# Performance work log

Hardware: AMD Instinct MI355X
Metric: run time of the kernel (lower is better)

The kernel has to match this reference:

```python
import jax, jax.numpy as jnp
import numpy as np

NHEADS = 16
LN_EPS = 1e-5


def setup_inputs() -> dict:
    key = jax.random.key(0)
    ks = jax.random.split(key, 12)
    B, L, D = 8, 1024, 1024
    bound = 1.0 / np.sqrt(D)
    inp = {
        'query': jax.random.normal(ks[0], (B, L, D), jnp.float32),
        'key':   jax.random.normal(ks[1], (B, L, D), jnp.float32),
        'value': jax.random.normal(ks[2], (B, L, D), jnp.float32),
        'q_mask': jnp.ones((B, L), jnp.float32),
        'k_mask': jnp.ones((B, L), jnp.float32),
        'Wq': jax.random.uniform(ks[3], (D, D), jnp.float32, -bound, bound),
        'bq': jax.random.uniform(ks[4], (D,), jnp.float32, -bound, bound),
        'Wk': jax.random.uniform(ks[5], (D, D), jnp.float32, -bound, bound),
        'bk': jax.random.uniform(ks[6], (D,), jnp.float32, -bound, bound),
        'Wv': jax.random.uniform(ks[7], (D, D), jnp.float32, -bound, bound),
        'bv': jax.random.uniform(ks[8], (D,), jnp.float32, -bound, bound),
        'Wo': jax.random.uniform(ks[9], (D, D), jnp.float32, -bound, bound),
        'bo': jax.random.uniform(ks[10], (D,), jnp.float32, -bound, bound),
        'gamma': jnp.ones((D,), jnp.float32),
        'beta': jnp.zeros((D,), jnp.float32),
    }
    return inp


def reference(query, key, value, q_mask, k_mask, Wq, bq, Wk, bk, Wv, bv, Wo, bo, gamma, beta):
    B, L, D = query.shape
    H = NHEADS
    d = D // H
    residual = query
    # linear projections (torch Linear: x @ W.T + b)
    q = query @ Wq.T + bq
    k = key @ Wk.T + bk
    v = value @ Wv.T + bv
    # NOTE: module does a raw contiguous view [B, L, H*d] -> [B*H, L, d]
    # (NOT a transpose-based head split). Replicate exactly.
    q = q.reshape(B * H, L, d)
    k = k.reshape(B * H, L, d)
    v = v.reshape(B * H, L, d)
    # masks tiled head-major: repeat(nheads, 1) -> [H*B, L]
    qm = jnp.tile(q_mask, (H, 1))
    km = jnp.tile(k_mask, (H, 1))
    mask = qm[:, :, None] * km[:, None, :]  # [B*H, L, L] outer product
    scores = jnp.einsum('bqd,bkd->bqk', q, k) / np.sqrt(d).astype(np.float32)
    A = jnp.exp(jnp.where(mask == 0, -jnp.inf, scores))  # unstable exp, as in source
    A_sum = jnp.clip(jnp.sum(A, axis=-1, keepdims=True), 2e-15, None)
    attn = A / A_sum
    context = (attn @ v).reshape(B, L, H * d)
    out = context @ Wo.T + bo
    # dropout is identity in eval mode
    x = residual + out
    mean = jnp.mean(x, axis=-1, keepdims=True)
    var = jnp.mean(jnp.square(x - mean), axis=-1, keepdims=True)
    return (x - mean) / jnp.sqrt(var + LN_EPS) * gamma + beta
```

## Files before the change

kernel.cpp:

```cpp
#include <hip/hip_runtime.h>
#include <hip/hip_bf16.h>


typedef __bf16 bf16x8 __attribute__((ext_vector_type(8)));
typedef float  f32x4  __attribute__((ext_vector_type(4)));

#define KK 1024
#define NN 1024

union BfPack4 { __bf16 h[4]; uint2 u; };
union BfPack8 { __bf16 h[8]; uint4 u; };

__device__ int g_nomask;

__device__ __forceinline__ void lds_copy16(void* lds, const void* gsrc) {
  __builtin_amdgcn_global_load_lds(
      (__attribute__((address_space(1))) void*)(uintptr_t)gsrc,
      (__attribute__((address_space(3))) void*)(unsigned int)(uintptr_t)lds,
      16, 0, 0);
}

struct Prep {
  const float* wsrc[4]; __bf16* wdst;
  const float* asrc[3]; __bf16* adst; int do_a;
  const float* qm; const float* km;
};

__global__ __launch_bounds__(256) void prep_kernel(Prep a) {
  const int bid = blockIdx.x;
  const int tid = threadIdx.x;
  if (bid < 12288) {
    if (!a.do_a) return;
    const int z = bid >> 12, i = bid & 4095;
    const float* s = a.asrc[z];
    __bf16* d = a.adst + (size_t)z * ((size_t)8 << 20);
    const size_t off = ((size_t)i * 256 + tid) * 8;
    float4 f0 = *(const float4*)&s[off];
    float4 f1 = *(const float4*)&s[off + 4];
    BfPack8 p;
    p.h[0] = (__bf16)f0.x; p.h[1] = (__bf16)f0.y;
    p.h[2] = (__bf16)f0.z; p.h[3] = (__bf16)f0.w;
    p.h[4] = (__bf16)f1.x; p.h[5] = (__bf16)f1.y;
    p.h[6] = (__bf16)f1.z; p.h[7] = (__bf16)f1.w;
    *(uint4*)&d[off] = p.u;
  } else if (bid < 16384) {
    const int b = bid - 12288;
    const int z = b >> 10, i = b & 1023;
    const float* s = a.wsrc[z];
    __bf16* d = a.wdst + (size_t)z * (KK * NN);
    const int idx = (i * 256 + tid) * 4;
    float4 f = *(const float4*)&s[idx];
    BfPack4 p;
    p.h[0] = (__bf16)f.x; p.h[1] = (__bf16)f.y;
    p.h[2] = (__bf16)f.z; p.h[3] = (__bf16)f.w;
    *(uint2*)&d[idx] = p.u;
  } else {
    int ok = 1;
    for (int i = tid; i < 8192; i += 256)
      ok &= (a.qm[i] != 0.f) & (a.km[i] != 0.f);
    const int all_ok = __syncthreads_and(ok);
    if (tid == 0) g_nomask = all_ok;
  }
}

struct G8 {
  const __bf16* A[3];
  const __bf16* W[3];
  const float*  bias[3];
  void*         C[3];
};

#define BAR()   __builtin_amdgcn_s_barrier()
#define PRIO(x) __builtin_amdgcn_s_setprio(x)
#define WAIT_LGKM0() do { asm volatile("s_waitcnt lgkmcnt(0)" ::: "memory"); \
                          __builtin_amdgcn_sched_barrier(0); } while (0)
#define WAIT_VM4()  asm volatile("s_waitcnt vmcnt(4)" ::: "memory")
#define WAIT_VM0()  asm volatile("s_waitcnt vmcnt(0)" ::: "memory")

#define STAGE_A(buf, half, kt) do {                                          \
  lds_copy16(smem + (buf)*32768 + (half)*16384 + ldsW,                       \
             pA0[half] + (size_t)(kt)*64);                                   \
  lds_copy16(smem + (buf)*32768 + (half)*16384 + ldsW + 1024,                \
             pA1[half] + (size_t)(kt)*64); } while (0)

#define STAGE_B(buf, half, kt) do {                                          \
  lds_copy16(smem + 65536 + (buf)*32768 + (half)*16384 + ldsW,               \
             pB0[half] + (size_t)(kt)*64);                                   \
  lds_copy16(smem + 65536 + (buf)*32768 + (half)*16384 + ldsW + 1024,        \
             pB1[half] + (size_t)(kt)*64); } while (0)

#define LDA(buf, mh) do {                                                    \
  const char* _p = aSelf + (buf)*32768 + (mh)*8192;                          \
  _Pragma("unroll") for (int i_ = 0; i_ < 4; ++i_) {                         \
    af[i_][0] = *(const bf16x8*)(_p + i_*2048 + c0_);                        \
    af[i_][1] = *(const bf16x8*)(_p + i_*2048 + c1_); } } while (0)

#define LDB(buf, nh) do {                                                    \
  const char* _p = bSelf + (buf)*32768 + (nh)*4096;                          \
  _Pragma("unroll") for (int j_ = 0; j_ < 2; ++j_) {                         \
    bf[(nh)*2 + j_][0] = *(const bf16x8*)(_p + j_*2048 + c0_);               \
    bf[(nh)*2 + j_][1] = *(const bf16x8*)(_p + j_*2048 + c1_); } } while (0)

#define MM(mh, nh) do {                                                      \
  _Pragma("unroll") for (int i_ = 0; i_ < 4; ++i_)                           \
  _Pragma("unroll") for (int j_ = 0; j_ < 2; ++j_) {                         \
    acc[(mh)*4+i_][(nh)*2+j_] = __builtin_amdgcn_mfma_f32_16x16x32_bf16(     \
        af[i_][0], bf[(nh)*2+j_][0], acc[(mh)*4+i_][(nh)*2+j_], 0, 0, 0);    \
    acc[(mh)*4+i_][(nh)*2+j_] = __builtin_amdgcn_mfma_f32_16x16x32_bf16(     \
        af[i_][1], bf[(nh)*2+j_][1], acc[(mh)*4+i_][(nh)*2+j_], 0, 0, 0);    \
  } } while (0)

template <bool OUT_BF16>
__global__ __launch_bounds__(512, 2) void gemm8p(G8 args)
{
  __shared__ __align__(16) char smem[131072];
  const int z = blockIdx.z;
  const __bf16* __restrict__ A    = args.A[z];
  const __bf16* __restrict__ W    = args.W[z];
  const float*  __restrict__ bias = args.bias[z];

  const int tid = threadIdx.x;
  const int l = tid & 63, w = tid >> 6;
  const int lr = l & 15, lq = l >> 4;
  const int wr = w >> 2, wc = w & 3;

  int lin = blockIdx.y * 32 + blockIdx.x;
  lin = (lin & 7) * 16 + (lin >> 3);
  const int m0 = (lin & 31) * 256;
  const int n0 = (lin >> 5) * 256;

  const int s0 = w * 128 + l, s1 = s0 + 64;
  const int r0 = s0 >> 3, kq0 = (s0 & 7) ^ (r0 & 7);
  const int r1 = s1 >> 3, kq1 = (s1 & 7) ^ (r1 & 7);
  const __bf16* pA0[2]; const __bf16* pA1[2];
  const __bf16* pB0[2]; const __bf16* pB1[2];
  #pragma unroll
  for (int h = 0; h < 2; ++h) {
    pA0[h] = A + (size_t)(m0 + h * 128 + r0) * KK + kq0 * 8;
    pA1[h] = A + (size_t)(m0 + h * 128 + r1) * KK + kq1 * 8;
    pB0[h] = W + (size_t)(n0 + h * 128 + r0) * KK + kq0 * 8;
    pB1[h] = W + (size_t)(n0 + h * 128 + r1) * KK + kq1 * 8;
  }
  const int ldsW = w * 2048;

  const int aRow = lr * 128;
  const int c0_ = ((lq)     ^ (lr & 7)) * 16;
  const int c1_ = ((4 + lq) ^ (lr & 7)) * 16;
  const char* aSelf = smem + wr * 16384 + aRow;
  const char* bSelf = smem + 65536 + (wc >> 1) * 16384 + (wc & 1) * 8192 + aRow;

  bf16x8 af[4][2], bf[4][2];
  f32x4 acc[8][4] = {};

  STAGE_A(0, 0, 0); STAGE_A(0, 1, 0);
  STAGE_B(0, 0, 0); STAGE_B(0, 1, 0);
  STAGE_B(1, 0, 1); STAGE_B(1, 1, 1);
  WAIT_VM4();
  BAR();

  for (int it = 0; it < 8; ++it) {
    const int t2 = it * 2;
    LDA(0, 0); LDB(0, 0);
    STAGE_A(1, 0, t2 + 1);
    BAR(); WAIT_LGKM0();
    PRIO(1); MM(0, 0); PRIO(0);
    BAR();
    LDB(0, 1);
    STAGE_A(1, 1, t2 + 1);
    BAR(); WAIT_LGKM0();
    PRIO(1); MM(0, 1); PRIO(0);
    BAR();
    LDA(0, 1);
    if (it < 7) STAGE_B(0, 0, t2 + 2);
    BAR(); WAIT_LGKM0();
    PRIO(1); MM(1, 0); PRIO(0);
    BAR();
    if (it < 7) { STAGE_B(0, 1, t2 + 2); WAIT_VM4(); }
    else        { WAIT_VM0(); }
    BAR();
    PRIO(1); MM(1, 1); PRIO(0);
    BAR();
    LDA(1, 0); LDB(1, 0);
    if (it < 7) STAGE_A(0, 0, t2 + 2);
    BAR(); WAIT_LGKM0();
    PRIO(1); MM(0, 0); PRIO(0);
    BAR();
    LDB(1, 1);
    if (it < 7) STAGE_A(0, 1, t2 + 2);
    BAR(); WAIT_LGKM0();
    PRIO(1); MM(0, 1); PRIO(0);
    BAR();
    LDA(1, 1);
    if (it < 7) STAGE_B(1, 0, t2 + 3);
    BAR(); WAIT_LGKM0();
    PRIO(1); MM(1, 0); PRIO(0);
    BAR();
    if (it < 7) { STAGE_B(1, 1, t2 + 3); WAIT_VM4(); }
    BAR();
    PRIO(1); MM(1, 1); PRIO(0);
    BAR();
  }

  float bv[4];
  #pragma unroll
  for (int n = 0; n < 4; ++n) bv[n] = bias[n0 + wc * 64 + n * 16 + lr];

  #pragma unroll
  for (int f = 0; f < 8; ++f) {
    const int gm = m0 + wr * 128 + f * 16 + lq * 4;
    #pragma unroll
    for (int n = 0; n < 4; ++n) {
      const int gn = n0 + wc * 64 + n * 16 + lr;
      #pragma unroll
      for (int i = 0; i < 4; ++i) {
        const float v = acc[f][n][i] + bv[n];
        if constexpr (OUT_BF16)
          ((__bf16*)args.C[z])[(size_t)(gm + i) * NN + gn] = (__bf16)v;
        else
          ((float*)args.C[z])[(size_t)(gm + i) * NN + gn] = v;
      }
    }
  }
}

struct GQKV {
  const float*  A[3];
  const __bf16* W;
  const float*  bias[3];
  __bf16*       C[3];
};

__global__ __launch_bounds__(256) void gemm_qkv(GQKV args)
{
  __shared__ alignas(16) __bf16 As[128 * 40];
  __shared__ alignas(16) __bf16 Bs[2][4096];
  const int z = blockIdx.z;
  const float*  A    = args.A[z];
  const __bf16* W    = args.W + (size_t)z * KK * NN;
  const float*  bias = args.bias[z];
  __bf16* C = args.C[z];
  const int tid = threadIdx.x, l = tid & 63, w = tid >> 6;
  const int m0 = blockIdx.x * 128, n0 = blockIdx.y * 128;
  const int lr = l & 15, lq = l >> 4;
  const int wm = (w & 1) * 64, wn = (w >> 1) * 64;

  const __bf16* gw0 = &W[(size_t)(n0 + (tid >> 2)) * KK + (tid & 3) * 8];
  const __bf16* gw1 = &W[(size_t)(n0 + 64 + (tid >> 2)) * KK + (tid & 3) * 8];

  float4 pa[4];
  #pragma unroll
  for (int s = 0; s < 4; ++s) {
    int c = tid + 256 * s; int row = c >> 3, ko = (c & 7) * 4;
    pa[s] = *(const float4*)&A[(size_t)(m0 + row) * KK + ko];
  }
  lds_copy16((char*)Bs + w * 1024,        gw0);
  lds_copy16((char*)Bs + 4096 + w * 1024, gw1);

  f32x4 acc[4][4] = {};
  int ib = 0;
  for (int kk = 0; kk < KK; kk += 32) {
    __syncthreads();
    #pragma unroll
    for (int s = 0; s < 4; ++s) {
      int c = tid + 256 * s; int row = c >> 3, ko = (c & 7) * 4;
      BfPack4 p;
      p.h[0] = (__bf16)pa[s].x; p.h[1] = (__bf16)pa[s].y;
      p.h[2] = (__bf16)pa[s].z; p.h[3] = (__bf16)pa[s].w;
      *(uint2*)&As[row * 40 + ko] = p.u;
    }
    __syncthreads();
    if (kk + 32 < KK) {
      lds_copy16((char*)Bs + (ib ^ 1) * 8192 + w * 1024,        gw0 + kk + 32);
      lds_copy16((char*)Bs + (ib ^ 1) * 8192 + 4096 + w * 1024, gw1 + kk + 32);
      #pragma unroll
      for (int s = 0; s < 4; ++s) {
        int c = tid + 256 * s; int row = c >> 3, ko = (c & 7) * 4;
        pa[s] = *(const float4*)&A[(size_t)(m0 + row) * KK + kk + 32 + ko];
      }
    }
    const __bf16* Bb = (const __bf16*)((char*)Bs + ib * 8192);
    bf16x8 af2[4], bf2[4];
    #pragma unroll
    for (int t = 0; t < 4; ++t) {
      af2[t] = *(const bf16x8*)&As[(wm + t * 16 + lr) * 40 + lq * 8];
      bf2[t] = *(const bf16x8*)&Bb[(wn + t * 16 + lr) * 32 + lq * 8];
    }
    #pragma unroll
    for (int mt = 0; mt < 4; ++mt)
      #pragma unroll
      for (int nt = 0; nt < 4; ++nt)
        acc[mt][nt] = __builtin_amdgcn_mfma_f32_16x16x32_bf16(af2[mt], bf2[nt], acc[mt][nt], 0, 0, 0);
    ib ^= 1;
  }

  #pragma unroll
  for (int mt = 0; mt < 4; ++mt)
    #pragma unroll
    for (int nt = 0; nt < 4; ++nt)
      #pragma unroll
      for (int i = 0; i < 4; ++i) {
        int gm = m0 + wm + mt * 16 + lq * 4 + i;
        int gn = n0 + wn + nt * 16 + lr;
        C[(size_t)gm * NN + gn] = (__bf16)(acc[mt][nt][i] + bias[gn]);
      }
}

__global__ __launch_bounds__(256) void attn_kernel(
    const __bf16* __restrict__ qb, const __bf16* __restrict__ kb,
    const __bf16* __restrict__ vb, const float* __restrict__ qm,
    const float* __restrict__ km, __bf16* __restrict__ ctxb)
{
  const int g  = blockIdx.x * 16 + (blockIdx.y >> 3);
  const int qt = blockIdx.y & 7;
  const int tid = threadIdx.x, l = tid & 63, w = tid >> 6;
  const int lr = l & 15, lq = l >> 4;

  __shared__ alignas(16) __bf16 Ps[128 * 64];
  __shared__ alignas(16) __bf16 Ks[2 * 128 * 32];
  __shared__ alignas(16) __bf16 Vt[64 * 128];
  __shared__ alignas(16) __bf16 kms[1024];

  const size_t gbase = (size_t)g * (1024 * 64);
  const __bf16* qg = qb + gbase;
  const __bf16* kg = kb + gbase;
  const __bf16* vg = vb + gbase;
  const float* qmrow = qm + (size_t)(g & 7) * 1024;
  const float* kmrow = km + (size_t)(g & 7) * 1024;
  const int nm = g_nomask;

  #pragma unroll
  for (int s = 0; s < 4; ++s) {
    int c = tid + 256 * s;
    int p = c >> 9, r = (c >> 2) & 127, q0 = c & 3;
    lds_copy16((char*)Ps + w * 1024 + s * 4096,
               &qg[(size_t)(qt * 128 + r) * 64 + p * 32 + q0 * 8]);
  }
  {
    float4 kf = *(const float4*)&kmrow[tid * 4];
    BfPack4 p;
    p.h[0] = (__bf16)(kf.x == 0.f ? 0.f : 1.f);
    p.h[1] = (__bf16)(kf.y == 0.f ? 0.f : 1.f);
    p.h[2] = (__bf16)(kf.z == 0.f ? 0.f : 1.f);
    p.h[3] = (__bf16)(kf.w == 0.f ? 0.f : 1.f);
    *(uint2*)&kms[tid * 4] = p.u;
  }
  float qmv[2][4];
  #pragma unroll
  for (int rt = 0; rt < 2; ++rt)
    #pragma unroll
    for (int i = 0; i < 4; ++i)
      qmv[rt][i] = qmrow[qt * 128 + 32 * w + rt * 16 + lq * 4 + i];

  int gkOff[4];
  #pragma unroll
  for (int s = 0; s < 4; ++s) {
    int c = tid + 256 * s;
    int p = c >> 9, r = (c >> 2) & 127, q0 = c & 3;
    gkOff[s] = r * 64 + p * 32 + ((q0 ^ (r & 3)) * 8);
  }

  __syncthreads();

  bf16x8 qa[2][2];
  #pragma unroll
  for (int rt = 0; rt < 2; ++rt)
    #pragma unroll
    for (int p = 0; p < 2; ++p)
      qa[rt][p] = *(const bf16x8*)((char*)Ps + p * 8192 +
                                   (32 * w + rt * 16 + lr) * 64 + lq * 16);

  uint4 pv[4];
  #pragma unroll
  for (int s = 0; s < 4; ++s) {
    int ch = tid + 256 * s; int j = ch & 127, c0 = ch >> 7;
    pv[s] = *(const uint4*)&vg[(size_t)j * 64 + c0 * 8];
  }

  const int kKey = (lq ^ (lr & 3)) << 4;
  const int pwKey = (lq << 1);
  const int prKey = ((lr >> 2) << 1);
  float rs[2][4] = {};
  f32x4 ctx[2][4] = {};

  for (int kt = 0; kt < 8; ++kt) {
    __syncthreads();
    #pragma unroll
    for (int s = 0; s < 4; ++s)
      lds_copy16((char*)Ks + w * 1024 + s * 4096,
                 kg + (size_t)kt * 8192 + gkOff[s]);
    #pragma unroll
    for (int s = 0; s < 4; ++s) {
      int ch = tid + 256 * s; int j = ch & 127, c0 = ch >> 7;
      BfPack8 vv; vv.u = pv[s];
      const int jhi = (j >> 3) << 4, jlo = (j & 7) * 2;
      #pragma unroll
      for (int cc = 0; cc < 8; ++cc) {
        int row = c0 * 8 + cc;
        *(__bf16*)((char*)Vt + row * 256 + (jhi ^ ((row & 15) << 4)) + jlo) =
            vv.h[cc];
      }
    }
    __syncthreads();
    if (kt < 7) {
      #pragma unroll
      for (int s = 0; s < 4; ++s) {
        int ch = tid + 256 * s; int j = ch & 127, c0 = ch >> 7;
        pv[s] = *(const uint4*)&vg[(size_t)((kt + 1) * 128 + j) * 64 + c0 * 8];
      }
    }
    #pragma unroll
    for (int h = 0; h < 2; ++h) {
      f32x4 sacc[2][4];
      PRIO(1);
      #pragma unroll
      for (int c4 = 0; c4 < 4; ++c4) {
        int ct = h * 4 + c4;
        bf16x8 kb0 = *(const bf16x8*)((char*)Ks + (ct * 16 + lr) * 64 + kKey);
        bf16x8 kb1 = *(const bf16x8*)((char*)Ks + 8192 + (ct * 16 + lr) * 64 + kKey);
        #pragma unroll
        for (int rt = 0; rt < 2; ++rt) {
          f32x4 zz = {};
          zz = __builtin_amdgcn_mfma_f32_16x16x32_bf16(qa[rt][0], kb0, zz, 0, 0, 0);
          sacc[rt][c4] = __builtin_amdgcn_mfma_f32_16x16x32_bf16(qa[rt][1], kb1, zz, 0, 0, 0);
        }
      }
      PRIO(0);
      if (nm) {
        #pragma unroll
        for (int c4 = 0; c4 < 4; ++c4)
          #pragma unroll
          for (int rt = 0; rt < 2; ++rt)
            #pragma unroll
            for (int i = 0; i < 4; ++i) {
              float e = __expf(sacc[rt][c4][i] * 0.125f);
              rs[rt][i] += e;
              int row = 32 * w + rt * 16 + lq * 4 + i;
              *(__bf16*)((char*)Ps + row * 128 +
                         (((c4 * 2 + (lr >> 3)) ^ pwKey) << 4) +
                         (lr & 7) * 2) = (__bf16)e;
            }
      } else {
        #pragma unroll
        for (int c4 = 0; c4 < 4; ++c4) {
          int ct = h * 4 + c4;
          float kmv = (float)kms[kt * 128 + ct * 16 + lr];
          #pragma unroll
          for (int rt = 0; rt < 2; ++rt)
            #pragma unroll
            for (int i = 0; i < 4; ++i) {
              float e = (qmv[rt][i] * kmv == 0.f) ? 0.f
                                                  : __expf(sacc[rt][c4][i] * 0.125f);
              rs[rt][i] += e;
              int row = 32 * w + rt * 16 + lq * 4 + i;
              *(__bf16*)((char*)Ps + row * 128 +
                         (((c4 * 2 + (lr >> 3)) ^ pwKey) << 4) +
                         (lr & 7) * 2) = (__bf16)e;
            }
        }
      }
      PRIO(1);
      #pragma unroll
      for (int ks = 0; ks < 2; ++ks) {
        bf16x8 pa2[2];
        #pragma unroll
        for (int rt = 0; rt < 2; ++rt) {
          int row = 32 * w + rt * 16 + lr;
          pa2[rt] = *(const bf16x8*)((char*)Ps + row * 128 +
                                     (((ks * 4 + lq) ^ prKey) << 4));
        }
        #pragma unroll
        for (int c2 = 0; c2 < 4; ++c2) {
          int vrow = c2 * 16 + lr;
          bf16x8 vf = *(const bf16x8*)((char*)Vt + vrow * 256 +
                        (((h * 8 + ks * 4 + lq) << 4) ^ ((vrow & 15) << 4)));
          #pragma unroll
          for (int rt = 0; rt < 2; ++rt)
            ctx[rt][c2] = __builtin_amdgcn_mfma_f32_16x16x32_bf16(pa2[rt], vf, ctx[rt][c2], 0, 0, 0);
        }
      }
      PRIO(0);
    }
  }

  #pragma unroll
  for (int rt = 0; rt < 2; ++rt)
    #pragma unroll
    for (int i = 0; i < 4; ++i) {
      float v = rs[rt][i];
      v += __shfl_xor(v, 1);
      v += __shfl_xor(v, 2);
      v += __shfl_xor(v, 4);
      v += __shfl_xor(v, 8);
      rs[rt][i] = 1.0f / fmaxf(v, 2e-15f);
    }

  #pragma unroll
  for (int rt = 0; rt < 2; ++rt)
    #pragma unroll
    for (int c2 = 0; c2 < 4; ++c2)
      #pragma unroll
      for (int i = 0; i < 4; ++i) {
        int row = qt * 128 + 32 * w + rt * 16 + lq * 4 + i;
        ctxb[gbase + (size_t)row * 64 + c2 * 16 + lr] =
            (__bf16)(ctx[rt][c2][i] * rs[rt][i]);
      }
}

__global__ __launch_bounds__(256) void ln_kernel(
    const float* __restrict__ O, const float* __restrict__ resid,
    const float* __restrict__ gam, const float* __restrict__ bet,
    float* __restrict__ out)
{
  const int row = blockIdx.x;
  const int tid = threadIdx.x;
  const float* orow = O + (size_t)row * 1024;
  const float* rrow = resid + (size_t)row * 1024;
  float x[4];
  float sum = 0.f, sq = 0.f;
  #pragma unroll
  for (int j = 0; j < 4; ++j) {
    int c = tid + j * 256;
    x[j] = orow[c] + rrow[c];
    sum += x[j];
    sq  += x[j] * x[j];
  }
  #pragma unroll
  for (int off = 32; off > 0; off >>= 1) {
    sum += __shfl_down(sum, off, 64);
    sq  += __shfl_down(sq, off, 64);
  }
  __shared__ float s1[4], s2[4];
  __shared__ float mean_s, inv_s;
  if ((tid & 63) == 0) { s1[tid >> 6] = sum; s2[tid >> 6] = sq; }
  __syncthreads();
  if (tid == 0) {
    float S = s1[0] + s1[1] + s1[2] + s1[3];
    float Q = s2[0] + s2[1] + s2[2] + s2[3];
    float mean = S * (1.0f / 1024.0f);
    float var  = fmaxf(Q * (1.0f / 1024.0f) - mean * mean, 0.0f);
    mean_s = mean;
    inv_s  = rsqrtf(var + 1e-5f);
  }
  __syncthreads();
  float mean = mean_s, inv = inv_s;
  #pragma unroll
  for (int j = 0; j < 4; ++j) {
    int c = tid + j * 256;
    out[(size_t)row * 1024 + c] = (x[j] - mean) * inv * gam[c] + bet[c];
  }
}

extern "C" void kernel_launch(void* const* d_in, const int* in_sizes, int n_in,
                              void* d_out, int out_size, void* d_ws, size_t ws_size,
                              hipStream_t stream)
{
  const float* query = (const float*)d_in[0];
  const float* keyi  = (const float*)d_in[1];
  const float* value = (const float*)d_in[2];
  const float* qmask = (const float*)d_in[3];
  const float* kmask = (const float*)d_in[4];
  const float* Wq = (const float*)d_in[5];
  const float* bq = (const float*)d_in[6];
  const float* Wk = (const float*)d_in[7];
  const float* bk = (const float*)d_in[8];
  const float* Wv = (const float*)d_in[9];
  const float* bv = (const float*)d_in[10];
  const float* Wo = (const float*)d_in[11];
  const float* bo = (const float*)d_in[12];
  const float* gam = (const float*)d_in[13];
  const float* bet = (const float*)d_in[14];

  char* ws = (char*)d_ws;
  __bf16* qbuf = (__bf16*)(ws);
  __bf16* kbuf = (__bf16*)(ws + ((size_t)16 << 20));
  __bf16* vbuf = (__bf16*)(ws + ((size_t)32 << 20));
  __bf16* wb   = (__bf16*)(ws + ((size_t)48 << 20));
  float*  obuf = (float*)(ws + ((size_t)16 << 20));
  __bf16* abuf = (__bf16*)(ws + ((size_t)56 << 20));

  const bool big = ws_size >= ((size_t)104 << 20);

  Prep pp;
  pp.wsrc[0] = Wq; pp.wsrc[1] = Wk; pp.wsrc[2] = Wv; pp.wsrc[3] = Wo;
  pp.wdst = wb;
  pp.asrc[0] = query; pp.asrc[1] = keyi; pp.asrc[2] = value;
  pp.adst = abuf; pp.do_a = big ? 1 : 0;
  pp.qm = qmask; pp.km = kmask;

  dim3 tb(256);
  hipLaunchKernelGGL(prep_kernel, dim3(16385), tb, 0, stream, pp);

  if (big) {
    G8 gq;
    gq.A[0] = abuf;
    gq.A[1] = abuf + ((size_t)8 << 20);
    gq.A[2] = abuf + ((size_t)16 << 20);
    gq.W[0] = wb; gq.W[1] = wb + (size_t)KK * NN; gq.W[2] = wb + (size_t)2 * KK * NN;
    gq.bias[0] = bq; gq.bias[1] = bk; gq.bias[2] = bv;
    gq.C[0] = qbuf; gq.C[1] = kbuf; gq.C[2] = vbuf;
    hipLaunchKernelGGL((gemm8p<true>), dim3(32, 4, 3), dim3(512), 0, stream, gq);
  } else {
    GQKV qkv;
    qkv.A[0] = query; qkv.A[1] = keyi; qkv.A[2] = value;
    qkv.W = wb;
    qkv.bias[0] = bq; qkv.bias[1] = bk; qkv.bias[2] = bv;
    qkv.C[0] = qbuf;  qkv.C[1] = kbuf; qkv.C[2] = vbuf;
    hipLaunchKernelGGL(gemm_qkv, dim3(64, 8, 3), tb, 0, stream, qkv);
  }

  hipLaunchKernelGGL(attn_kernel, dim3(8, 128), tb, 0, stream,
                     qbuf, kbuf, vbuf, qmask, kmask, qbuf);

  G8 go;
  go.A[0] = qbuf;
  go.W[0] = wb + (size_t)3 * KK * NN;
  go.bias[0] = bo;
  go.C[0] = obuf;
  go.A[1] = go.A[2] = go.A[0]; go.W[1] = go.W[2] = go.W[0];
  go.bias[1] = go.bias[2] = go.bias[0]; go.C[1] = go.C[2] = go.C[0];
  hipLaunchKernelGGL((gemm8p<false>), dim3(32, 4, 1), dim3(512), 0, stream, go);

  hipLaunchKernelGGL(ln_kernel, dim3(8192), tb, 0, stream,
                     obuf, query, gam, bet, (float*)d_out);
}
```

Before: 353.7 us.

## Double-buffer K tiles and transpose QK^T MFMA for packed P stores

The attention kernel now keeps two K tiles in LDS and issues the async global-to-LDS load for the next tile before computing on the current one, so the K load overlaps compute instead of sitting between barriers. It also swaps the MFMA operands so each lane holds scores along a query row. That lets the softmax exponents be packed four at a time into a single 8-byte LDS store with a new XOR swizzle, and row sums finish with two cross-lane shuffles plus a broadcast. The cost is twice the LDS for K, which may lower occupancy.

```diff
diff --git a/kernel.cpp b/kernel.cpp
--- a/kernel.cpp
+++ b/kernel.cpp
@@ -316,7 +316,7 @@
   const int lr = l & 15, lq = l >> 4;
 
   __shared__ alignas(16) __bf16 Ps[128 * 64];
-  __shared__ alignas(16) __bf16 Ks[2 * 128 * 32];
+  __shared__ alignas(16) __bf16 Ks[2][8192];
   __shared__ alignas(16) __bf16 Vt[64 * 128];
   __shared__ alignas(16) __bf16 kms[1024];
 
@@ -344,12 +344,10 @@
     p.h[3] = (__bf16)(kf.w == 0.f ? 0.f : 1.f);
     *(uint2*)&kms[tid * 4] = p.u;
   }
-  float qmv[2][4];
+  float qmv2[2];
   #pragma unroll
   for (int rt = 0; rt < 2; ++rt)
-    #pragma unroll
-    for (int i = 0; i < 4; ++i)
-      qmv[rt][i] = qmrow[qt * 128 + 32 * w + rt * 16 + lq * 4 + i];
+    qmv2[rt] = qmrow[qt * 128 + 32 * w + rt * 16 + lr];
 
   int gkOff[4];
   #pragma unroll
@@ -358,6 +356,9 @@
     int p = c >> 9, r = (c >> 2) & 127, q0 = c & 3;
     gkOff[s] = r * 64 + p * 32 + ((q0 ^ (r & 3)) * 8);
   }
+  #pragma unroll
+  for (int s = 0; s < 4; ++s)
+    lds_copy16((char*)Ks + w * 1024 + s * 4096, kg + gkOff[s]);
 
   __syncthreads();
 
@@ -377,17 +378,12 @@
   }
 
   const int kKey = (lq ^ (lr & 3)) << 4;
-  const int pwKey = (lq << 1);
-  const int prKey = ((lr >> 2) << 1);
-  float rs[2][4] = {};
+  float rs[2] = {};
   f32x4 ctx[2][4] = {};
 
   for (int kt = 0; kt < 8; ++kt) {
+    const int buf = kt & 1;
     __syncthreads();
-    #pragma unroll
-    for (int s = 0; s < 4; ++s)
-      lds_copy16((char*)Ks + w * 1024 + s * 4096,
-                 kg + (size_t)kt * 8192 + gkOff[s]);
     #pragma unroll
     for (int s = 0; s < 4; ++s) {
       int ch = tid + 256 * s; int j = ch & 127, c0 = ch >> 7;
@@ -403,11 +399,16 @@
     __syncthreads();
     if (kt < 7) {
       #pragma unroll
+      for (int s = 0; s < 4; ++s)
+        lds_copy16((char*)Ks + (buf ^ 1) * 16384 + w * 1024 + s * 4096,
+                   kg + (size_t)(kt + 1) * 8192 + gkOff[s]);
+      #pragma unroll
       for (int s = 0; s < 4; ++s) {
         int ch = tid + 256 * s; int j = ch & 127, c0 = ch >> 7;
         pv[s] = *(const uint4*)&vg[(size_t)((kt + 1) * 128 + j) * 64 + c0 * 8];
       }
     }
+    const char* Kb = (const char*)Ks + buf * 16384;
     #pragma unroll
     for (int h = 0; h < 2; ++h) {
       f32x4 sacc[2][4];
@@ -415,47 +416,40 @@
       #pragma unroll
       for (int c4 = 0; c4 < 4; ++c4) {
         int ct = h * 4 + c4;
-        bf16x8 kb0 = *(const bf16x8*)((char*)Ks + (ct * 16 + lr) * 64 + kKey);
-        bf16x8 kb1 = *(const bf16x8*)((char*)Ks + 8192 + (ct * 16 + lr) * 64 + kKey);
+        bf16x8 kb0 = *(const bf16x8*)(Kb + (ct * 16 + lr) * 64 + kKey);
+        bf16x8 kb1 = *(const bf16x8*)(Kb + 8192 + (ct * 16 + lr) * 64 + kKey);
         #pragma unroll
         for (int rt = 0; rt < 2; ++rt) {
           f32x4 zz = {};
-          zz = __builtin_amdgcn_mfma_f32_16x16x32_bf16(qa[rt][0], kb0, zz, 0, 0, 0);
-          sacc[rt][c4] = __builtin_amdgcn_mfma_f32_16x16x32_bf16(qa[rt][1], kb1, zz, 0, 0, 0);
+          zz = __builtin_amdgcn_mfma_f32_16x16x32_bf16(kb0, qa[rt][0], zz, 0, 0, 0);
+          sacc[rt][c4] = __builtin_amdgcn_mfma_f32_16x16x32_bf16(kb1, qa[rt][1], sacc[rt][c4] = zz, 0, 0, 0);
         }
       }
       PRIO(0);
-      if (nm) {
+      #pragma unroll
+      for (int c4 = 0; c4 < 4; ++c4) {
+        BfPack4 km4;
+        if (!nm)
+          km4.u = *(const uint2*)&kms[kt * 128 + h * 64 + c4 * 16 + lq * 4];
         #pragma unroll
-        for (int c4 = 0; c4 < 4; ++c4)
+        for (int rt = 0; rt < 2; ++rt) {
+          BfPack4 pk4;
           #pragma unroll
-          for (int rt = 0; rt < 2; ++rt)
-            #pragma unroll
-            for (int i = 0; i < 4; ++i) {
-              float e = __expf(sacc[rt][c4][i] * 0.125f);
-              rs[rt][i] += e;
-              int row = 32 * w + rt * 16 + lq * 4 + i;
-              *(__bf16*)((char*)Ps + row * 128 +
-                         (((c4 * 2 + (lr >> 3)) ^ pwKey) << 4) +
-                         (lr & 7) * 2) = (__bf16)e;
+          for (int i = 0; i < 4; ++i) {
+            float e;
+            if (nm) {
+              e = __expf(sacc[rt][c4][i] * 0.125f);
+            } else {
+              float kmv = (float)km4.h[i];
+              e = (qmv2[rt] * kmv == 0.f) ? 0.f
+                                          : __expf(sacc[rt][c4][i] * 0.125f);
             }
-      } else {
-        #pragma unroll
-        for (int c4 = 0; c4 < 4; ++c4) {
-          int ct = h * 4 + c4;
-          float kmv = (float)kms[kt * 128 + ct * 16 + lr];
-          #pragma unroll
-          for (int rt = 0; rt < 2; ++rt)
-            #pragma unroll
-            for (int i = 0; i < 4; ++i) {
-              float e = (qmv[rt][i] * kmv == 0.f) ? 0.f
-                                                  : __expf(sacc[rt][c4][i] * 0.125f);
-              rs[rt][i] += e;
-              int row = 32 * w + rt * 16 + lq * 4 + i;
-              *(__bf16*)((char*)Ps + row * 128 +
-                         (((c4 * 2 + (lr >> 3)) ^ pwKey) << 4) +
-                         (lr & 7) * 2) = (__bf16)e;
-            }
+            rs[rt] += e;
+            pk4.h[i] = (__bf16)e;
+          }
+          const int row = 32 * w + rt * 16 + lr;
+          const int gp = (2 * c4 + (lq >> 1)) ^ (lr & 7);
+          *(uint2*)((char*)Ps + row * 128 + (gp << 4) + (lq & 1) * 8) = pk4.u;
         }
       }
       PRIO(1);
@@ -464,9 +458,9 @@
         bf16x8 pa2[2];
         #pragma unroll
         for (int rt = 0; rt < 2; ++rt) {
-          int row = 32 * w + rt * 16 + lr;
+          const int row = 32 * w + rt * 16 + lr;
           pa2[rt] = *(const bf16x8*)((char*)Ps + row * 128 +
-                                     (((ks * 4 + lq) ^ prKey) << 4));
+                                     (((ks * 4 + lq) ^ (lr & 7)) << 4));
         }
         #pragma unroll
         for (int c2 = 0; c2 < 4; ++c2) {
@@ -482,17 +476,20 @@
     }
   }
 
+  float rsum[2];
+  #pragma unroll
+  for (int rt = 0; rt < 2; ++rt) {
+    float v = rs[rt];
+    v += __shfl_xor(v, 16);
+    v += __shfl_xor(v, 32);
+    rsum[rt] = 1.0f / fmaxf(v, 2e-15f);
+  }
+  float rinv[2][4];
   #pragma unroll
   for (int rt = 0; rt < 2; ++rt)
     #pragma unroll
-    for (int i = 0; i < 4; ++i) {
-      float v = rs[rt][i];
-      v += __shfl_xor(v, 1);
-      v += __shfl_xor(v, 2);
-      v += __shfl_xor(v, 4);
-      v += __shfl_xor(v, 8);
-      rs[rt][i] = 1.0f / fmaxf(v, 2e-15f);
-    }
+    for (int i = 0; i < 4; ++i)
+      rinv[rt][i] = __shfl(rsum[rt], lq * 4 + i, 64);
 
   #pragma unroll
   for (int rt = 0; rt < 2; ++rt)
@@ -502,7 +499,7 @@
       for (int i = 0; i < 4; ++i) {
         int row = qt * 128 + 32 * w + rt * 16 + lq * 4 + i;
         ctxb[gbase + (size_t)row * 64 + c2 * 16 + lr] =
-            (__bf16)(ctx[rt][c2][i] * rs[rt][i]);
+            (__bf16)(ctx[rt][c2][i] * rinv[rt][i]);
       }
 }
 
```

Result: slower. 367.7 us (+4.0%).
